# Performance work log

Hardware: AMD Instinct MI355X
Metric: run time of the kernel (lower is better)

Reference implementation:

```python
import jax, jax.numpy as jnp
import numpy as np

N, E, G = 50000, 500000, 2048
HID, H, ED, L = 128, 4, 12, 8
D = HID // H
EPS_BN = 1e-5


def setup_inputs() -> dict:
    key = jax.random.key(0)
    ks = jax.random.split(key, 32)
    s = 0.05
    x = jax.random.normal(ks[0], (N, 22), jnp.float32)
    src = jax.random.randint(ks[1], (E,), 0, N)
    off = jax.random.randint(ks[2], (E,), 1, N)
    dst = (src + off) % N  # guaranteed no self-loops -> move_mask is all True
    batch = jnp.sort(jax.random.randint(ks[3], (N,), 0, G))
    edge_attr = jax.random.normal(ks[4], (E, ED), jnp.float32)
    params = dict(
        Win=jax.random.normal(ks[5], (22, HID), jnp.float32) * s,
        b_in=jnp.zeros((HID,), jnp.float32),
        Wl=jax.random.normal(ks[6], (L, HID, HID), jnp.float32) * s,
        bl=jnp.zeros((L, HID), jnp.float32),
        Wr=jax.random.normal(ks[7], (L, HID, HID), jnp.float32) * s,
        br=jnp.zeros((L, HID), jnp.float32),
        We=jax.random.normal(ks[8], (L, ED, HID), jnp.float32) * s,
        att=jax.random.normal(ks[9], (L, H, D), jnp.float32) * s,
        bo=jnp.zeros((L, HID), jnp.float32),
        gamma=jnp.ones((L, HID), jnp.float32),
        beta=jnp.zeros((L, HID), jnp.float32),
        Wv1=jax.random.normal(ks[10], (HID, 64), jnp.float32) * s,
        bv1=jnp.zeros((64,), jnp.float32),
        Wv2=jax.random.normal(ks[11], (64, 3), jnp.float32) * s,
        bv2=jnp.zeros((3,), jnp.float32),
        Wp1=jax.random.normal(ks[12], (2 * HID + ED, 64), jnp.float32) * s,
        bp1=jnp.zeros((64,), jnp.float32),
        Wp2=jax.random.normal(ks[13], (64, 1), jnp.float32) * s,
        bp2=jnp.zeros((1,), jnp.float32),
    )
    return dict(x=x, src=src, dst=dst, batch=batch, edge_attr=edge_attr, **params)


def _bn(h, g, b):
    mu = h.mean(0)
    var = h.var(0)
    return (h - mu) * jax.lax.rsqrt(var + EPS_BN) * g + b


def _gatv2(h, src, dst, edge_attr, Wl, bl, Wr, br, We, att, bo):
    xl = (h @ Wl + bl).reshape(N, H, D)   # source-side (values + score)
    xr = (h @ Wr + br).reshape(N, H, D)   # target-side (score)
    e = (edge_attr @ We).reshape(E, H, D)
    sc = xl[src] + xr[dst] + e            # [E,H,D]
    sc = jnp.where(sc > 0, sc, 0.2 * sc)  # LeakyReLU(0.2)
    a = jnp.einsum('ehd,hd->eh', sc, att)  # [E,H]
    m = jax.ops.segment_max(a, dst, num_segments=N)
    ex = jnp.exp(a - m[dst])
    den = jax.ops.segment_sum(ex, dst, num_segments=N)
    alpha = ex / (den[dst] + 1e-16)        # per-destination softmax
    out = jax.ops.segment_sum(xl[src] * alpha[..., None], dst, num_segments=N)
    return out.reshape(N, HID) + bo


def reference(x, src, dst, batch, edge_attr, Win, b_in, Wl, bl, Wr, br, We, att,
              bo, gamma, beta, Wv1, bv1, Wv2, bv2, Wp1, bp1, Wp2, bp2):
    h = jax.nn.relu(x @ Win + b_in)
    for blk in range(L // 2):
        i, j = 2 * blk, 2 * blk + 1
        res = h
        h = jax.nn.relu(_bn(_gatv2(h, src, dst, edge_attr, Wl[i], bl[i], Wr[i], br[i], We[i], att[i], bo[i]), gamma[i], beta[i]))
        h = _bn(_gatv2(h, src, dst, edge_attr, Wl[j], bl[j], Wr[j], br[j], We[j], att[j], bo[j]), gamma[j], beta[j])
        h = jax.nn.relu(h + res)
    cnt = jax.ops.segment_sum(jnp.ones((N,), h.dtype), batch, num_segments=G)
    pooled = jax.ops.segment_sum(h, batch, num_segments=G) / jnp.maximum(cnt, 1.0)[:, None]
    value_logits = jax.nn.relu(pooled @ Wv1 + bv1) @ Wv2 + bv2   # [G,3]
    edge_in = jnp.concatenate([h[src], h[dst], edge_attr], axis=1)  # [E, 2*HID+ED]
    policy_logits = (jax.nn.relu(edge_in @ Wp1 + bp1) @ Wp2 + bp2)[:, 0]  # [E]
    return (value_logits, policy_logits)
```

## Files before the change

kernel.cpp:

```cpp
#include <hip/hip_runtime.h>
#include <math.h>

#define N_NODES 50000
#define N_EDGES 500000
#define N_GRAPHS 2048
#define HID 128
#define EDIM 12
#define NLAYERS 8
#define EPS_BN 1e-5f
#define LOG2E 1.44269504088896340736f

typedef __attribute__((ext_vector_type(8))) short short8;
typedef __attribute__((ext_vector_type(4))) float f32x4;
typedef __attribute__((ext_vector_type(2))) float f32x2;
typedef unsigned int uint;
typedef unsigned short ushort;

__device__ inline ushort f2bf(float x) {
  unsigned u = __float_as_uint(x);
  u = (u + 0x7FFFu + ((u >> 16) & 1u)) >> 16;
  return (ushort)u;
}
__device__ inline unsigned pk_bf16(float a, float b) {
  return (unsigned)f2bf(a) | ((unsigned)f2bf(b) << 16);
}
__device__ inline float bflo(uint q) { return __uint_as_float(q << 16); }
__device__ inline float bfhi(uint q) { return __uint_as_float(q & 0xFFFF0000u); }
__device__ inline f32x2 pfma(f32x2 a, f32x2 b, f32x2 c) {
  return __builtin_elementwise_fma(a, b, c);
}
template <int CTRL>
__device__ inline float dpp_add(float v) {
  int s = __builtin_amdgcn_update_dpp(0, __float_as_int(v), CTRL, 0xF, 0xF, true);
  return v + __int_as_float(s);
}
#define RED16(v)              \
  v = dpp_add<0xB1>(v);       \
  v = dpp_add<0x4E>(v);       \
  v = dpp_add<0x141>(v);      \
  v = dpp_add<0x140>(v);

__global__ void zero_kernel(int* deg, int* cursor, float* stats, uint* erec) {
  int i = blockIdx.x * 256 + threadIdx.x;
  if (i < N_NODES) { deg[i] = 0; cursor[i] = 0; }
  if (i < NLAYERS * 256) stats[i] = 0.f;
  if (i < 32) erec[(size_t)N_EDGES * 8 + i] = 0u;
}

__global__ void count_kernel(const int* __restrict__ dst, int* __restrict__ deg) {
  int e = blockIdx.x * 256 + threadIdx.x;
  if (e < N_EDGES) atomicAdd(&deg[dst[e]], 1);
}

__global__ void scan1_kernel(int* __restrict__ off, int* __restrict__ bsum) {
  __shared__ int s[256];
  int t = threadIdx.x; int n = blockIdx.x * 256 + t;
  int x = (n < N_NODES) ? off[n] : 0;
  s[t] = x; __syncthreads();
  for (int o = 1; o < 256; o <<= 1) {
    int v = (t >= o) ? s[t - o] : 0;
    __syncthreads(); s[t] += v; __syncthreads();
  }
  if (n < N_NODES) off[n] = s[t] - x;
  if (t == 255) bsum[blockIdx.x] = s[255];
}

__global__ void scan2_kernel(int* __restrict__ bsum, int nb) {
  __shared__ int s[256];
  int t = threadIdx.x;
  int x = (t < nb) ? bsum[t] : 0;
  s[t] = x; __syncthreads();
  for (int o = 1; o < 256; o <<= 1) {
    int v = (t >= o) ? s[t - o] : 0;
    __syncthreads(); s[t] += v; __syncthreads();
  }
  if (t < nb) bsum[t] = s[t] - x;
}

__global__ void scan3_kernel(int* __restrict__ off, const int* __restrict__ bsum) {
  int t = threadIdx.x; int n = blockIdx.x * 256 + t;
  if (n < N_NODES) off[n] += bsum[blockIdx.x];
  if (n == 0 && blockIdx.x == 0) off[N_NODES] = N_EDGES;
}

__global__ void scatter_kernel(const int* __restrict__ src, const int* __restrict__ dst,
                               const float* __restrict__ ea,
                               const int* __restrict__ off, int* __restrict__ cursor,
                               uint* __restrict__ erec) {
  int e = blockIdx.x * 256 + threadIdx.x;
  if (e < N_EDGES) {
    int d = dst[e];
    int p = atomicAdd(&cursor[d], 1);
    int pos = off[d] + p;
    const float* eap = &ea[(size_t)e * EDIM];
    float4 e0 = *(const float4*)eap;
    float4 e1 = *(const float4*)(eap + 4);
    float4 e2 = *(const float4*)(eap + 8);
    uint4 q0, q1;
    q0.x = (uint)src[e]; q0.y = 0u;
    q0.z = pk_bf16(e0.x, e0.y); q0.w = pk_bf16(e0.z, e0.w);
    q1.x = pk_bf16(e1.x, e1.y); q1.y = pk_bf16(e1.z, e1.w);
    q1.z = pk_bf16(e2.x, e2.y); q1.w = pk_bf16(e2.z, e2.w);
    uint* o = &erec[(size_t)pos * 8];
    *(uint4*)o = q0;
    *(uint4*)(o + 4) = q1;
  }
}

__global__ void wprep_kernel(const float* __restrict__ Wl, const float* __restrict__ Wr,
                             ushort* __restrict__ wpk) {
  int idx = blockIdx.x * 256 + threadIdx.x;
  if (idx >= NLAYERS * 4 * 256 * 32) return;
  int kk = idx & 31;
  int cc = (idx >> 5) & 255;
  int kb = (idx >> 13) & 3;
  int layer = idx >> 15;
  int k = kb * 32 + kk;
  float v = (cc < 128) ? Wl[((size_t)layer * 128 + k) * 128 + cc]
                       : Wr[((size_t)layer * 128 + k) * 128 + (cc - 128)];
  wpk[idx] = f2bf(v);
}

__global__ void wprep_pol_kernel(const float* __restrict__ Wp1, ushort* __restrict__ wppk) {
  int idx = blockIdx.x * 256 + threadIdx.x;
  if (idx >= 4 * 128 * 32) return;
  int kk = idx & 31;
  int cc = (idx >> 5) & 127;
  int kb = idx >> 12;
  int k = kb * 32 + kk;
  float v = (cc < 64) ? Wp1[(size_t)k * 64 + cc] : Wp1[(size_t)(128 + k) * 64 + (cc - 64)];
  wppk[idx] = f2bf(v);
}

__global__ void inproj_kernel(const float* __restrict__ x, const float* __restrict__ Win,
                              const float* __restrict__ b_in, float* __restrict__ h,
                              ushort* __restrict__ h16) {
  __shared__ float xs[44];
  int t = threadIdx.x;
  int n0 = blockIdx.x * 2;
  if (t < 44) xs[t] = x[n0 * 22 + t];
  __syncthreads();
  int c = t & 127, half = t >> 7;
  int n = n0 + half;
  if (n < N_NODES) {
    float acc = b_in[c];
#pragma unroll
    for (int k = 0; k < 22; k++) acc = fmaf(xs[half * 22 + k], Win[k * HID + c], acc);
    float v = fmaxf(acc, 0.f);
    h[(size_t)n * HID + c] = v;
    h16[(size_t)n * HID + c] = f2bf(v);
  }
}

template <int NOUT, int SPLIT, bool BIAS, bool OUTBF16, bool BNFUSE, bool RESID, bool WRITEH>
__global__ __launch_bounds__(256) void gemm_mfma_kernel(
    const ushort* __restrict__ A16, const ushort* __restrict__ T16,
    const float* __restrict__ stats, const float* __restrict__ gamma,
    const float* __restrict__ beta, const float* __restrict__ res,
    float* __restrict__ hout,
    const ushort* __restrict__ Wpk, const float* __restrict__ b1,
    const float* __restrict__ b2, void* __restrict__ C1v, void* __restrict__ C2v,
    int nrows) {
  __shared__ ushort As[64][136];
  int t = threadIdx.x;
  int brow = blockIdx.x * 64;
  if constexpr (!BNFUSE) {
#pragma unroll
    for (int i = 0; i < 4; i++) {
      int f = t + i * 256;
      int r = f >> 4, cg = (f & 15) * 8;
      int g = brow + r;
      uint4 v = make_uint4(0, 0, 0, 0);
      if (g < nrows) v = *(const uint4*)&A16[(size_t)g * HID + cg];
      *(uint4*)&As[r][cg] = v;
    }
  } else {
    int cg = (t & 31) * 4;
    int r0 = t >> 5;
    const float invN = 1.f / (float)N_NODES;
    float4 sm = *(const float4*)&stats[cg];
    float4 sq = *(const float4*)&stats[128 + cg];
    float4 gm = *(const float4*)&gamma[cg];
    float4 bt = *(const float4*)&beta[cg];
    float s4[4] = {sm.x, sm.y, sm.z, sm.w};
    float q4[4] = {sq.x, sq.y, sq.z, sq.w};
    float g4[4] = {gm.x, gm.y, gm.z, gm.w};
    float bb4[4] = {bt.x, bt.y, bt.z, bt.w};
    float scl[4], shf[4];
#pragma unroll
    for (int k = 0; k < 4; k++) {
      float mu = s4[k] * invN;
      float var = q4[k] * invN - mu * mu;
      float rs = rsqrtf(var + EPS_BN);
      scl[k] = g4[k] * rs;
      shf[k] = bb4[k] - mu * scl[k];
    }
#pragma unroll
    for (int rr = 0; rr < 8; rr++) {
      int r = r0 + rr * 8;
      int g = brow + r;
      uint2 tvu = make_uint2(0u, 0u);
      if (g < nrows) tvu = *(const uint2*)&T16[(size_t)g * HID + cg];
      float o0 = fmaf(bflo(tvu.x), scl[0], shf[0]);
      float o1 = fmaf(bfhi(tvu.x), scl[1], shf[1]);
      float o2 = fmaf(bflo(tvu.y), scl[2], shf[2]);
      float o3 = fmaf(bfhi(tvu.y), scl[3], shf[3]);
      if constexpr (RESID) {
        if (g < nrows) {
          float4 rv = *(const float4*)&res[(size_t)g * HID + cg];
          o0 += rv.x; o1 += rv.y; o2 += rv.z; o3 += rv.w;
        }
      }
      o0 = fmaxf(o0, 0.f); o1 = fmaxf(o1, 0.f);
      o2 = fmaxf(o2, 0.f); o3 = fmaxf(o3, 0.f);
      if constexpr (WRITEH) {
        if (g < nrows) {
          float4 ov = make_float4(o0, o1, o2, o3);
          *(float4*)&hout[(size_t)g * HID + cg] = ov;
        }
      }
      *(uint2*)&As[r][cg] = make_uint2(pk_bf16(o0, o1), pk_bf16(o2, o3));
    }
  }
  __syncthreads();
  int lane = t & 63, wave = t >> 6;
  int arow = wave * 16 + (lane & 15);
  int k8 = (lane >> 4) * 8;
  constexpr int NT = NOUT / 16;
  f32x4 acc[NT];
#pragma unroll
  for (int n = 0; n < NT; n++) acc[n] = (f32x4){0.f, 0.f, 0.f, 0.f};
#pragma unroll
  for (int kb = 0; kb < 4; kb++) {
    short8 a = *(const short8*)&As[arow][kb * 32 + k8];
#pragma unroll
    for (int n = 0; n < NT; n++) {
      int col = n * 16 + (lane & 15);
      short8 b = *(const short8*)&Wpk[((size_t)(kb * NOUT + col)) * 32 + k8];
      acc[n] = __builtin_amdgcn_mfma_f32_16x16x32_bf16(a, b, acc[n], 0, 0, 0);
    }
  }
  int rbase = brow + wave * 16 + (lane >> 4) * 4;
  int ccol = lane & 15;
#pragma unroll
  for (int n = 0; n < NT; n++) {
    int col = n * 16 + ccol;
    float bias = 0.f;
    if (BIAS) bias = (col < SPLIT) ? b1[col] : b2[col - SPLIT];
    int colw = (col < SPLIT) ? col : col - SPLIT;
#pragma unroll
    for (int j = 0; j < 4; j++) {
      int row = rbase + j;
      if (row < nrows) {
        float v = acc[n][j] + bias;
        if (OUTBF16) {
          ushort* dstp = (ushort*)((col < SPLIT) ? C1v : C2v);
          dstp[(size_t)row * SPLIT + colw] = f2bf(v);
        } else {
          float* dstp = (float*)((col < SPLIT) ? C1v : C2v);
          dstp[(size_t)row * SPLIT + colw] = v;
        }
      }
    }
  }
}

#define GAT_EDGE(ra, rb, xlw, m, d, acc)                                    \
  {                                                                         \
    f32x2 xa = (f32x2){bflo(xlw), bfhi(xlw)};                               \
    f32x2 ep = xa + xrv;                                                    \
    uint q;                                                                 \
    q = ra.z;                                                               \
    ep = pfma((f32x2){bflo(q), bflo(q)}, wk[0], ep);                        \
    ep = pfma((f32x2){bfhi(q), bfhi(q)}, wk[1], ep);                        \
    q = ra.w;                                                               \
    ep = pfma((f32x2){bflo(q), bflo(q)}, wk[2], ep);                        \
    ep = pfma((f32x2){bfhi(q), bfhi(q)}, wk[3], ep);                        \
    q = rb.x;                                                               \
    ep = pfma((f32x2){bflo(q), bflo(q)}, wk[4], ep);                        \
    ep = pfma((f32x2){bfhi(q), bfhi(q)}, wk[5], ep);                        \
    q = rb.y;                                                               \
    ep = pfma((f32x2){bflo(q), bflo(q)}, wk[6], ep);                        \
    ep = pfma((f32x2){bfhi(q), bfhi(q)}, wk[7], ep);                        \
    q = rb.z;                                                               \
    ep = pfma((f32x2){bflo(q), bflo(q)}, wk[8], ep);                        \
    ep = pfma((f32x2){bfhi(q), bfhi(q)}, wk[9], ep);                        \
    q = rb.w;                                                               \
    ep = pfma((f32x2){bflo(q), bflo(q)}, wk[10], ep);                       \
    ep = pfma((f32x2){bfhi(q), bfhi(q)}, wk[11], ep);                       \
    f32x2 sv = __builtin_elementwise_max(ep, ep * (f32x2){0.2f, 0.2f});     \
    float v = fmaf(sv.y, at.y, sv.x * at.x);                                \
    RED16(v)                                                                \
    float dm = v - m;                                                       \
    float e = __builtin_amdgcn_exp2f(-fabsf(dm));                           \
    bool big = dm > 0.f;                                                    \
    float sc = big ? e : 1.f;                                               \
    float p = big ? 1.f : e;                                                \
    m = fmaxf(m, v);                                                        \
    d = fmaf(d, sc, p);                                                     \
    acc = pfma(acc, (f32x2){sc, sc}, (f32x2){p, p} * xa);                   \
  }

__global__ __launch_bounds__(256, 4) void gat_kernel(
    const ushort* __restrict__ xl16, const ushort* __restrict__ xr16,
    const uint* __restrict__ erec, const int* __restrict__ off,
    const float* __restrict__ Wel, const float* __restrict__ attl,
    const float* __restrict__ bol, ushort* __restrict__ out16) {
  int lane = threadIdx.x & 63;
  int node = blockIdx.x * 4 + (threadIdx.x >> 6);
  if (node >= N_NODES) return;
  int c0 = lane * 2;

  f32x2 wk[12];
#pragma unroll
  for (int k = 0; k < 12; k++) {
    float2 w = *(const float2*)&Wel[k * HID + c0];
    wk[k] = (f32x2){w.x, w.y};
  }
  float2 at = *(const float2*)&attl[c0];
  at.x *= LOG2E; at.y *= LOG2E;
  uint xrd = *(const uint*)&xr16[((uint)node << 7) + c0];
  f32x2 xrv = (f32x2){bflo(xrd), bfhi(xrd)};

  int is = off[node], deg = off[node + 1] - is;
  const uint* p = erec + (size_t)is * 8;

  float m0 = -INFINITY, d0 = 0.f;
  float m1 = -INFINITY, d1 = 0.f;
  f32x2 acc0 = (f32x2){0.f, 0.f};
  f32x2 acc1 = (f32x2){0.f, 0.f};

  if (deg > 0) {
    uint4 Aa = *(const uint4*)p,        Ab = *(const uint4*)(p + 4);
    uint4 Ba = *(const uint4*)(p + 8),  Bb = *(const uint4*)(p + 12);
    uint xA = *(const uint*)&xl16[(Aa.x << 7) + c0];
    int i = 0;
    for (; i + 2 <= deg; i += 2) {
      uint xB = *(const uint*)&xl16[(Ba.x << 7) + c0];
      const uint* q2 = p + (size_t)(i + 2) * 8;
      uint4 Ca = *(const uint4*)q2,        Cb = *(const uint4*)(q2 + 4);
      uint4 Da = *(const uint4*)(q2 + 8),  Db = *(const uint4*)(q2 + 12);
      GAT_EDGE(Aa, Ab, xA, m0, d0, acc0)
      uint xC = *(const uint*)&xl16[(Ca.x << 7) + c0];
      GAT_EDGE(Ba, Bb, xB, m1, d1, acc1)
      Aa = Ca; Ab = Cb; Ba = Da; Bb = Db; xA = xC;
    }
    if (i < deg) GAT_EDGE(Aa, Ab, xA, m0, d0, acc0)
  }
  float mn = fmaxf(m0, m1);
  float w0 = (m0 > -INFINITY) ? __builtin_amdgcn_exp2f(m0 - mn) : 0.f;
  float w1 = (m1 > -INFINITY) ? __builtin_amdgcn_exp2f(m1 - mn) : 0.f;
  float den = d0 * w0 + d1 * w1;
  f32x2 acc = acc0 * (f32x2){w0, w0} + acc1 * (f32x2){w1, w1};
  float inv = 1.f / (den + 1e-16f);
  float2 bo2 = *(const float2*)&bol[c0];
  out16[((uint)node << 7) + c0 + 0] = f2bf(fmaf(acc.x, inv, bo2.x));
  out16[((uint)node << 7) + c0 + 1] = f2bf(fmaf(acc.y, inv, bo2.y));
}

__global__ void bnstats_kernel(const ushort* __restrict__ t16, float* __restrict__ sums) {
  int tid = threadIdx.x;
  int c2 = (tid & 63) * 2;
  int grp = tid >> 6;
  float s0 = 0.f, s1 = 0.f, q0 = 0.f, q1 = 0.f;
  for (int n = blockIdx.x * 4 + grp; n < N_NODES; n += 1024) {
    uint v = *(const uint*)&t16[((uint)n << 7) + c2];
    float a = bflo(v), b = bfhi(v);
    s0 += a; q0 = fmaf(a, a, q0);
    s1 += b; q1 = fmaf(b, b, q1);
  }
  __shared__ float ls[4][128], lq[4][128];
  *(float2*)&ls[grp][c2] = make_float2(s0, s1);
  *(float2*)&lq[grp][c2] = make_float2(q0, q1);
  __syncthreads();
  if (tid < 128) {
    float s = ls[0][tid] + ls[1][tid] + ls[2][tid] + ls[3][tid];
    atomicAdd(&sums[tid], s);
    float q = lq[0][tid] + lq[1][tid] + lq[2][tid] + lq[3][tid];
    atomicAdd(&sums[128 + tid], q);
  }
}

__global__ __launch_bounds__(256) void policy_kernel(
    const ushort* __restrict__ Ps, const ushort* __restrict__ Pd,
    const int* __restrict__ src, const int* __restrict__ dst,
    const float* __restrict__ edge_attr, const float* __restrict__ Wp1e,
    const float* __restrict__ bp1, const float* __restrict__ Wp2,
    const float* __restrict__ bp2, float* __restrict__ outp) {
  int lane = threadIdx.x & 63;
  int j = lane & 15;
  int e = (blockIdx.x * 256 + threadIdx.x) >> 4;
  if (e >= N_EDGES) return;
  float4 we[12];
#pragma unroll
  for (int k = 0; k < 12; k++) we[k] = *(const float4*)&Wp1e[k * 64 + j * 4];
  float4 b4 = *(const float4*)&bp1[j * 4];
  float4 w2 = *(const float4*)&Wp2[j * 4];
  float bp2c = bp2[0];
  int s = src[e], d = dst[e];
  const float* eap = &edge_attr[(size_t)e * EDIM];
  float4 e0 = *(const float4*)eap;
  float4 e1 = *(const float4*)(eap + 4);
  float4 e2 = *(const float4*)(eap + 8);
  uint2 psu = *(const uint2*)&Ps[(size_t)s * 64 + j * 4];
  uint2 pdu = *(const uint2*)&Pd[(size_t)d * 64 + j * 4];
  float eav[12] = {e0.x, e0.y, e0.z, e0.w, e1.x, e1.y, e1.z, e1.w, e2.x, e2.y, e2.z, e2.w};
  float hx = bflo(psu.x) + bflo(pdu.x) + b4.x;
  float hy = bfhi(psu.x) + bfhi(pdu.x) + b4.y;
  float hz = bflo(psu.y) + bflo(pdu.y) + b4.z;
  float hw = bfhi(psu.y) + bfhi(pdu.y) + b4.w;
#pragma unroll
  for (int k = 0; k < 12; k++) {
    hx = fmaf(eav[k], we[k].x, hx);
    hy = fmaf(eav[k], we[k].y, hy);
    hz = fmaf(eav[k], we[k].z, hz);
    hw = fmaf(eav[k], we[k].w, hw);
  }
  hx = fmaxf(hx, 0.f); hy = fmaxf(hy, 0.f); hz = fmaxf(hz, 0.f); hw = fmaxf(hw, 0.f);
  float v = fmaf(hx, w2.x, fmaf(hy, w2.y, fmaf(hz, w2.z, hw * w2.w)));
  v += __shfl_xor(v, 1);
  v += __shfl_xor(v, 2);
  v += __shfl_xor(v, 4);
  v += __shfl_xor(v, 8);
  if (j == 0) outp[e] = v + bp2c;
}

__device__ int lower_bound_dev(const int* a, int n, int key) {
  int lo = 0, hi = n;
  while (lo < hi) {
    int mid = (lo + hi) >> 1;
    if (a[mid] < key) lo = mid + 1; else hi = mid;
  }
  return lo;
}

__global__ void poolvalue_kernel(const float* __restrict__ h, const int* __restrict__ batch,
                                 const float* __restrict__ Wv1, const float* __restrict__ bv1,
                                 const float* __restrict__ Wv2, const float* __restrict__ bv2,
                                 float* __restrict__ outv) {
  __shared__ float pl[128];
  __shared__ float hd[64];
  __shared__ int range[2];
  int g = blockIdx.x, t = threadIdx.x;
  if (t == 0) {
    range[0] = lower_bound_dev(batch, N_NODES, g);
    range[1] = lower_bound_dev(batch, N_NODES, g + 1);
  }
  __syncthreads();
  int lo = range[0], hi = range[1];
  float s = 0.f;
  for (int n = lo; n < hi; n++) s += h[(size_t)n * HID + t];
  float cnt = (float)(hi - lo);
  pl[t] = s / fmaxf(cnt, 1.f);
  __syncthreads();
  if (t < 64) {
    float a = bv1[t];
    for (int c = 0; c < 128; c++) a = fmaf(pl[c], Wv1[c * 64 + t], a);
    hd[t] = fmaxf(a, 0.f);
  }
  __syncthreads();
  if (t < 3) {
    float a = bv2[t];
    for (int j = 0; j < 64; j++) a = fmaf(hd[j], Wv2[j * 3 + t], a);
    outv[g * 3 + t] = a;
  }
}

extern "C" void kernel_launch(void* const* d_in, const int* in_sizes, int n_in,
                              void* d_out, int out_size, void* d_ws, size_t ws_size,
                              hipStream_t stream) {
  (void)in_sizes; (void)n_in; (void)out_size; (void)ws_size;
  const float* x    = (const float*)d_in[0];
  const int*   src  = (const int*)d_in[1];
  const int*   dst  = (const int*)d_in[2];
  const int*   batch= (const int*)d_in[3];
  const float* ea   = (const float*)d_in[4];
  const float* Win  = (const float*)d_in[5];
  const float* b_in = (const float*)d_in[6];
  const float* Wl   = (const float*)d_in[7];
  const float* bl   = (const float*)d_in[8];
  const float* Wr   = (const float*)d_in[9];
  const float* br   = (const float*)d_in[10];
  const float* We   = (const float*)d_in[11];
  const float* att  = (const float*)d_in[12];
  const float* bo   = (const float*)d_in[13];
  const float* gamma= (const float*)d_in[14];
  const float* beta = (const float*)d_in[15];
  const float* Wv1  = (const float*)d_in[16];
  const float* bv1  = (const float*)d_in[17];
  const float* Wv2  = (const float*)d_in[18];
  const float* bv2  = (const float*)d_in[19];
  const float* Wp1  = (const float*)d_in[20];
  const float* bp1  = (const float*)d_in[21];
  const float* Wp2  = (const float*)d_in[22];
  const float* bp2  = (const float*)d_in[23];

  float* outv = (float*)d_out;
  float* outp = outv + (size_t)N_GRAPHS * 3;

  float* hres   = (float*)d_ws;
  ushort* tmp16 = (ushort*)(hres + (size_t)N_NODES * HID);
  ushort* h16   = tmp16 + (size_t)N_NODES * HID;
  ushort* xl16  = h16 + (size_t)N_NODES * HID;
  ushort* xr16  = xl16 + (size_t)N_NODES * HID;
  float* stats  = (float*)(xr16 + (size_t)N_NODES * HID);
  ushort* wpk   = (ushort*)(stats + NLAYERS * 256);
  ushort* wppk  = wpk + (size_t)NLAYERS * 4 * 256 * 32;
  int* off    = (int*)(wppk + 4 * 128 * 32);
  int* cursor = off + (N_NODES + 1);
  int* bsum   = cursor + N_NODES;
  uint* erec  = (uint*)(((uintptr_t)(bsum + 256) + 15) & ~(uintptr_t)15);

  const int NB = (N_NODES + 255) / 256;
  const int EB = (N_EDGES + 255) / 256;

  zero_kernel<<<NB, 256, 0, stream>>>(off, cursor, stats, erec);
  count_kernel<<<EB, 256, 0, stream>>>(dst, off);
  scan1_kernel<<<NB, 256, 0, stream>>>(off, bsum);
  scan2_kernel<<<1, 256, 0, stream>>>(bsum, NB);
  scan3_kernel<<<NB, 256, 0, stream>>>(off, bsum);
  scatter_kernel<<<EB, 256, 0, stream>>>(src, dst, ea, off, cursor, erec);
  wprep_kernel<<<(NLAYERS * 4 * 256 * 32 + 255) / 256, 256, 0, stream>>>(Wl, Wr, wpk);
  wprep_pol_kernel<<<(4 * 128 * 32 + 255) / 256, 256, 0, stream>>>(Wp1, wppk);
  inproj_kernel<<<N_NODES / 2, 256, 0, stream>>>(x, Win, b_in, hres, h16);

  const int MB = (N_NODES + 63) / 64;
  const int GATB = (N_NODES + 3) / 4;

  for (int l = 0; l < NLAYERS; l++) {
    if (l == 0) {
      gemm_mfma_kernel<256, 128, true, true, false, false, false><<<MB, 256, 0, stream>>>(
          h16, nullptr, nullptr, nullptr, nullptr, nullptr, nullptr,
          wpk, bl, br, xl16, xr16, N_NODES);
    } else if (l & 1) {
      int p = l - 1;
      gemm_mfma_kernel<256, 128, true, true, true, false, false><<<MB, 256, 0, stream>>>(
          nullptr, tmp16, stats + p * 256, gamma + p * HID, beta + p * HID, nullptr, nullptr,
          wpk + (size_t)l * 32768, bl + l * HID, br + l * HID, xl16, xr16, N_NODES);
    } else {
      int p = l - 1;
      gemm_mfma_kernel<256, 128, true, true, true, true, true><<<MB, 256, 0, stream>>>(
          nullptr, tmp16, stats + p * 256, gamma + p * HID, beta + p * HID, hres, hres,
          wpk + (size_t)l * 32768, bl + l * HID, br + l * HID, xl16, xr16, N_NODES);
    }
    gat_kernel<<<GATB, 256, 0, stream>>>(xl16, xr16, erec, off,
                                         We + (size_t)l * EDIM * HID, att + (size_t)l * HID,
                                         bo + (size_t)l * HID, tmp16);
    bnstats_kernel<<<256, 256, 0, stream>>>(tmp16, stats + l * 256);
  }

  ushort* Ps = xl16;
  ushort* Pd = xr16;
  gemm_mfma_kernel<128, 64, false, true, true, true, true><<<MB, 256, 0, stream>>>(
      nullptr, tmp16, stats + 7 * 256, gamma + 7 * HID, beta + 7 * HID, hres, hres,
      wppk, nullptr, nullptr, Ps, Pd, N_NODES);
  policy_kernel<<<(N_EDGES + 15) / 16, 256, 0, stream>>>(Ps, Pd, src, dst, ea,
                                                         Wp1 + 256 * 64, bp1, Wp2, bp2, outp);
  poolvalue_kernel<<<N_GRAPHS, 128, 0, stream>>>(hres, batch, Wv1, bv1, Wv2, bv2, outv);
}
```

Baseline: 1.296 ms.

## Split GAT edges across wavefront halves and make policy kernel grid-stride

The GAT aggregation kernel now gives each half of a 64-lane wavefront a separate edge stream (even and odd edges). Each lane handles four channels instead of two, and the two partial online-softmax states are merged with cross-half shuffles at the end. This halves the per-node serial edge loop and shortens the attention-score reduction to 8 lanes, at the cost of more registers per lane and a masked tail edge. Separately, the policy kernel becomes a persistent grid-stride loop over 2048 blocks, so the per-thread weight loads are amortised across many edges.

```diff
diff --git a/kernel.cpp b/kernel.cpp
--- a/kernel.cpp
+++ b/kernel.cpp
@@ -34,11 +34,10 @@
   int s = __builtin_amdgcn_update_dpp(0, __float_as_int(v), CTRL, 0xF, 0xF, true);
   return v + __int_as_float(s);
 }
-#define RED16(v)              \
+#define RED8(v)               \
   v = dpp_add<0xB1>(v);       \
   v = dpp_add<0x4E>(v);       \
-  v = dpp_add<0x141>(v);      \
-  v = dpp_add<0x140>(v);
+  v = dpp_add<0x141>(v);
 
 __global__ void zero_kernel(int* deg, int* cursor, float* stats, uint* erec) {
   int i = blockIdx.x * 256 + threadIdx.x;
@@ -265,40 +264,58 @@
   }
 }
 
-#define GAT_EDGE(ra, rb, xlw, m, d, acc)                                    \
-  {                                                                         \
-    f32x2 xa = (f32x2){bflo(xlw), bfhi(xlw)};                               \
-    f32x2 ep = xa + xrv;                                                    \
-    uint q;                                                                 \
-    q = ra.z;                                                               \
-    ep = pfma((f32x2){bflo(q), bflo(q)}, wk[0], ep);                        \
-    ep = pfma((f32x2){bfhi(q), bfhi(q)}, wk[1], ep);                        \
-    q = ra.w;                                                               \
-    ep = pfma((f32x2){bflo(q), bflo(q)}, wk[2], ep);                        \
-    ep = pfma((f32x2){bfhi(q), bfhi(q)}, wk[3], ep);                        \
-    q = rb.x;                                                               \
-    ep = pfma((f32x2){bflo(q), bflo(q)}, wk[4], ep);                        \
-    ep = pfma((f32x2){bfhi(q), bfhi(q)}, wk[5], ep);                        \
-    q = rb.y;                                                               \
-    ep = pfma((f32x2){bflo(q), bflo(q)}, wk[6], ep);                        \
-    ep = pfma((f32x2){bfhi(q), bfhi(q)}, wk[7], ep);                        \
-    q = rb.z;                                                               \
-    ep = pfma((f32x2){bflo(q), bflo(q)}, wk[8], ep);                        \
-    ep = pfma((f32x2){bfhi(q), bfhi(q)}, wk[9], ep);                        \
-    q = rb.w;                                                               \
-    ep = pfma((f32x2){bflo(q), bflo(q)}, wk[10], ep);                       \
-    ep = pfma((f32x2){bfhi(q), bfhi(q)}, wk[11], ep);                       \
-    f32x2 sv = __builtin_elementwise_max(ep, ep * (f32x2){0.2f, 0.2f});     \
-    float v = fmaf(sv.y, at.y, sv.x * at.x);                                \
-    RED16(v)                                                                \
-    float dm = v - m;                                                       \
-    float e = __builtin_amdgcn_exp2f(-fabsf(dm));                           \
-    bool big = dm > 0.f;                                                    \
-    float sc = big ? e : 1.f;                                               \
-    float p = big ? 1.f : e;                                                \
-    m = fmaxf(m, v);                                                        \
-    d = fmaf(d, sc, p);                                                     \
-    acc = pfma(acc, (f32x2){sc, sc}, (f32x2){p, p} * xa);                   \
+#define GAT_EDGE4(ra, rb, xw, OKEXPR)                                        \
+  {                                                                          \
+    f32x2 xa01 = (f32x2){bflo(xw.x), bfhi(xw.x)};                            \
+    f32x2 xa23 = (f32x2){bflo(xw.y), bfhi(xw.y)};                            \
+    f32x2 ep01 = xa01 + xr01;                                                \
+    f32x2 ep23 = xa23 + xr23;                                                \
+    uint q; float lo, hi;                                                    \
+    q = ra.z; lo = bflo(q); hi = bfhi(q);                                    \
+    ep01 = pfma((f32x2){lo, lo}, wk01[0], ep01);                             \
+    ep23 = pfma((f32x2){lo, lo}, wk23[0], ep23);                             \
+    ep01 = pfma((f32x2){hi, hi}, wk01[1], ep01);                             \
+    ep23 = pfma((f32x2){hi, hi}, wk23[1], ep23);                             \
+    q = ra.w; lo = bflo(q); hi = bfhi(q);                                    \
+    ep01 = pfma((f32x2){lo, lo}, wk01[2], ep01);                             \
+    ep23 = pfma((f32x2){lo, lo}, wk23[2], ep23);                             \
+    ep01 = pfma((f32x2){hi, hi}, wk01[3], ep01);                             \
+    ep23 = pfma((f32x2){hi, hi}, wk23[3], ep23);                             \
+    q = rb.x; lo = bflo(q); hi = bfhi(q);                                    \
+    ep01 = pfma((f32x2){lo, lo}, wk01[4], ep01);                             \
+    ep23 = pfma((f32x2){lo, lo}, wk23[4], ep23);                             \
+    ep01 = pfma((f32x2){hi, hi}, wk01[5], ep01);                             \
+    ep23 = pfma((f32x2){hi, hi}, wk23[5], ep23);                             \
+    q = rb.y; lo = bflo(q); hi = bfhi(q);                                    \
+    ep01 = pfma((f32x2){lo, lo}, wk01[6], ep01);                             \
+    ep23 = pfma((f32x2){lo, lo}, wk23[6], ep23);                             \
+    ep01 = pfma((f32x2){hi, hi}, wk01[7], ep01);                             \
+    ep23 = pfma((f32x2){hi, hi}, wk23[7], ep23);                             \
+    q = rb.z; lo = bflo(q); hi = bfhi(q);                                    \
+    ep01 = pfma((f32x2){lo, lo}, wk01[8], ep01);                             \
+    ep23 = pfma((f32x2){lo, lo}, wk23[8], ep23);                             \
+    ep01 = pfma((f32x2){hi, hi}, wk01[9], ep01);                             \
+    ep23 = pfma((f32x2){hi, hi}, wk23[9], ep23);                             \
+    q = rb.w; lo = bflo(q); hi = bfhi(q);                                    \
+    ep01 = pfma((f32x2){lo, lo}, wk01[10], ep01);                            \
+    ep23 = pfma((f32x2){lo, lo}, wk23[10], ep23);                            \
+    ep01 = pfma((f32x2){hi, hi}, wk01[11], ep01);                            \
+    ep23 = pfma((f32x2){hi, hi}, wk23[11], ep23);                            \
+    f32x2 s01 = __builtin_elementwise_max(ep01, ep01 * (f32x2){0.2f, 0.2f}); \
+    f32x2 s23 = __builtin_elementwise_max(ep23, ep23 * (f32x2){0.2f, 0.2f}); \
+    float v = fmaf(s01.x, at4.x,                                             \
+              fmaf(s01.y, at4.y, fmaf(s23.x, at4.z, s23.y * at4.w)));        \
+    RED8(v)                                                                  \
+    bool ok = (OKEXPR);                                                      \
+    float dm = v - m;                                                        \
+    float e = __builtin_amdgcn_exp2f(-fabsf(dm));                            \
+    bool big = dm > 0.f;                                                     \
+    float sc = (big && ok) ? e : 1.f;                                        \
+    float p = ok ? (big ? 1.f : e) : 0.f;                                    \
+    m = (ok && big) ? v : m;                                                 \
+    d = fmaf(d, sc, p);                                                      \
+    acc01 = pfma(acc01, (f32x2){sc, sc}, (f32x2){p, p} * xa01);              \
+    acc23 = pfma(acc23, (f32x2){sc, sc}, (f32x2){p, p} * xa23);              \
   }
 
 __global__ __launch_bounds__(256, 4) void gat_kernel(
@@ -309,53 +326,62 @@
   int lane = threadIdx.x & 63;
   int node = blockIdx.x * 4 + (threadIdx.x >> 6);
   if (node >= N_NODES) return;
-  int c0 = lane * 2;
-
-  f32x2 wk[12];
+  int half = lane >> 5;
+  int c0 = (lane & 31) * 4;
+
+  f32x2 wk01[12], wk23[12];
 #pragma unroll
   for (int k = 0; k < 12; k++) {
-    float2 w = *(const float2*)&Wel[k * HID + c0];
-    wk[k] = (f32x2){w.x, w.y};
-  }
-  float2 at = *(const float2*)&attl[c0];
-  at.x *= LOG2E; at.y *= LOG2E;
-  uint xrd = *(const uint*)&xr16[((uint)node << 7) + c0];
-  f32x2 xrv = (f32x2){bflo(xrd), bfhi(xrd)};
+    float4 w = *(const float4*)&Wel[k * HID + c0];
+    wk01[k] = (f32x2){w.x, w.y};
+    wk23[k] = (f32x2){w.z, w.w};
+  }
+  float4 at4 = *(const float4*)&attl[c0];
+  at4.x *= LOG2E; at4.y *= LOG2E; at4.z *= LOG2E; at4.w *= LOG2E;
+  uint2 xru = *(const uint2*)&xr16[((uint)node << 7) + c0];
+  f32x2 xr01 = (f32x2){bflo(xru.x), bfhi(xru.x)};
+  f32x2 xr23 = (f32x2){bflo(xru.y), bfhi(xru.y)};
 
   int is = off[node], deg = off[node + 1] - is;
-  const uint* p = erec + (size_t)is * 8;
-
-  float m0 = -INFINITY, d0 = 0.f;
-  float m1 = -INFINITY, d1 = 0.f;
-  f32x2 acc0 = (f32x2){0.f, 0.f};
-  f32x2 acc1 = (f32x2){0.f, 0.f};
+
+  float m = -INFINITY, d = 0.f;
+  f32x2 acc01 = (f32x2){0.f, 0.f};
+  f32x2 acc23 = (f32x2){0.f, 0.f};
 
   if (deg > 0) {
-    uint4 Aa = *(const uint4*)p,        Ab = *(const uint4*)(p + 4);
-    uint4 Ba = *(const uint4*)(p + 8),  Bb = *(const uint4*)(p + 12);
-    uint xA = *(const uint*)&xl16[(Aa.x << 7) + c0];
-    int i = 0;
-    for (; i + 2 <= deg; i += 2) {
-      uint xB = *(const uint*)&xl16[(Ba.x << 7) + c0];
-      const uint* q2 = p + (size_t)(i + 2) * 8;
-      uint4 Ca = *(const uint4*)q2,        Cb = *(const uint4*)(q2 + 4);
-      uint4 Da = *(const uint4*)(q2 + 8),  Db = *(const uint4*)(q2 + 12);
-      GAT_EDGE(Aa, Ab, xA, m0, d0, acc0)
-      uint xC = *(const uint*)&xl16[(Ca.x << 7) + c0];
-      GAT_EDGE(Ba, Bb, xB, m1, d1, acc1)
-      Aa = Ca; Ab = Cb; Ba = Da; Bb = Db; xA = xC;
-    }
-    if (i < deg) GAT_EDGE(Aa, Ab, xA, m0, d0, acc0)
-  }
-  float mn = fmaxf(m0, m1);
-  float w0 = (m0 > -INFINITY) ? __builtin_amdgcn_exp2f(m0 - mn) : 0.f;
-  float w1 = (m1 > -INFINITY) ? __builtin_amdgcn_exp2f(m1 - mn) : 0.f;
-  float den = d0 * w0 + d1 * w1;
-  f32x2 acc = acc0 * (f32x2){w0, w0} + acc1 * (f32x2){w1, w1};
+    const uint* pe = erec + ((size_t)is + half) * 8;
+    uint4 Ra = *(const uint4*)pe, Rb = *(const uint4*)(pe + 4);
+    uint2 xw = *(const uint2*)&xl16[(Ra.x << 7) + c0];
+    int full = deg >> 1;
+    for (int i = 0; i < full; i++) {
+      const uint* pn = pe + 16;
+      uint4 Na = *(const uint4*)pn, Nb = *(const uint4*)(pn + 4);
+      uint2 xn = *(const uint2*)&xl16[(Na.x << 7) + c0];
+      GAT_EDGE4(Ra, Rb, xw, true)
+      Ra = Na; Rb = Nb; xw = xn; pe = pn;
+    }
+    if (deg & 1) GAT_EDGE4(Ra, Rb, xw, half == 0)
+  }
+
+  float mo = __shfl_xor(m, 32);
+  float dd = __shfl_xor(d, 32);
+  f32x2 o01, o23;
+  o01.x = __shfl_xor(acc01.x, 32); o01.y = __shfl_xor(acc01.y, 32);
+  o23.x = __shfl_xor(acc23.x, 32); o23.y = __shfl_xor(acc23.y, 32);
+  float mn = fmaxf(m, mo);
+  float wS = (m > -INFINITY) ? __builtin_amdgcn_exp2f(m - mn) : 0.f;
+  float wO = (mo > -INFINITY) ? __builtin_amdgcn_exp2f(mo - mn) : 0.f;
+  float den = d * wS + dd * wO;
+  f32x2 a01 = acc01 * (f32x2){wS, wS} + o01 * (f32x2){wO, wO};
+  f32x2 a23 = acc23 * (f32x2){wS, wS} + o23 * (f32x2){wO, wO};
   float inv = 1.f / (den + 1e-16f);
-  float2 bo2 = *(const float2*)&bol[c0];
-  out16[((uint)node << 7) + c0 + 0] = f2bf(fmaf(acc.x, inv, bo2.x));
-  out16[((uint)node << 7) + c0 + 1] = f2bf(fmaf(acc.y, inv, bo2.y));
+  if (half == 0) {
+    float4 bo = *(const float4*)&bol[c0];
+    uint2 o;
+    o.x = pk_bf16(fmaf(a01.x, inv, bo.x), fmaf(a01.y, inv, bo.y));
+    o.y = pk_bf16(fmaf(a23.x, inv, bo.z), fmaf(a23.y, inv, bo.w));
+    *(uint2*)&out16[((uint)node << 7) + c0] = o;
+  }
 }
 
 __global__ void bnstats_kernel(const ushort* __restrict__ t16, float* __restrict__ sums) {
@@ -387,42 +413,43 @@
     const float* __restrict__ edge_attr, const float* __restrict__ Wp1e,
     const float* __restrict__ bp1, const float* __restrict__ Wp2,
     const float* __restrict__ bp2, float* __restrict__ outp) {
-  int lane = threadIdx.x & 63;
-  int j = lane & 15;
-  int e = (blockIdx.x * 256 + threadIdx.x) >> 4;
-  if (e >= N_EDGES) return;
+  int j = threadIdx.x & 15;
+  int gid = (blockIdx.x * 256 + threadIdx.x) >> 4;
+  int ngroups = (gridDim.x * 256) >> 4;
   float4 we[12];
 #pragma unroll
   for (int k = 0; k < 12; k++) we[k] = *(const float4*)&Wp1e[k * 64 + j * 4];
   float4 b4 = *(const float4*)&bp1[j * 4];
   float4 w2 = *(const float4*)&Wp2[j * 4];
   float bp2c = bp2[0];
-  int s = src[e], d = dst[e];
-  const float* eap = &edge_attr[(size_t)e * EDIM];
-  float4 e0 = *(const float4*)eap;
-  float4 e1 = *(const float4*)(eap + 4);
-  float4 e2 = *(const float4*)(eap + 8);
-  uint2 psu = *(const uint2*)&Ps[(size_t)s * 64 + j * 4];
-  uint2 pdu = *(const uint2*)&Pd[(size_t)d * 64 + j * 4];
-  float eav[12] = {e0.x, e0.y, e0.z, e0.w, e1.x, e1.y, e1.z, e1.w, e2.x, e2.y, e2.z, e2.w};
-  float hx = bflo(psu.x) + bflo(pdu.x) + b4.x;
-  float hy = bfhi(psu.x) + bfhi(pdu.x) + b4.y;
-  float hz = bflo(psu.y) + bflo(pdu.y) + b4.z;
-  float hw = bfhi(psu.y) + bfhi(pdu.y) + b4.w;
-#pragma unroll
-  for (int k = 0; k < 12; k++) {
-    hx = fmaf(eav[k], we[k].x, hx);
-    hy = fmaf(eav[k], we[k].y, hy);
-    hz = fmaf(eav[k], we[k].z, hz);
-    hw = fmaf(eav[k], we[k].w, hw);
-  }
-  hx = fmaxf(hx, 0.f); hy = fmaxf(hy, 0.f); hz = fmaxf(hz, 0.f); hw = fmaxf(hw, 0.f);
-  float v = fmaf(hx, w2.x, fmaf(hy, w2.y, fmaf(hz, w2.z, hw * w2.w)));
-  v += __shfl_xor(v, 1);
-  v += __shfl_xor(v, 2);
-  v += __shfl_xor(v, 4);
-  v += __shfl_xor(v, 8);
-  if (j == 0) outp[e] = v + bp2c;
+  for (int e = gid; e < N_EDGES; e += ngroups) {
+    int s = src[e], d = dst[e];
+    const float* eap = &edge_attr[(size_t)e * EDIM];
+    float4 e0 = *(const float4*)eap;
+    float4 e1 = *(const float4*)(eap + 4);
+    float4 e2 = *(const float4*)(eap + 8);
+    uint2 psu = *(const uint2*)&Ps[(size_t)s * 64 + j * 4];
+    uint2 pdu = *(const uint2*)&Pd[(size_t)d * 64 + j * 4];
+    float eav[12] = {e0.x, e0.y, e0.z, e0.w, e1.x, e1.y, e1.z, e1.w, e2.x, e2.y, e2.z, e2.w};
+    float hx = bflo(psu.x) + bflo(pdu.x) + b4.x;
+    float hy = bfhi(psu.x) + bfhi(pdu.x) + b4.y;
+    float hz = bflo(psu.y) + bflo(pdu.y) + b4.z;
+    float hw = bfhi(psu.y) + bfhi(pdu.y) + b4.w;
+#pragma unroll
+    for (int k = 0; k < 12; k++) {
+      hx = fmaf(eav[k], we[k].x, hx);
+      hy = fmaf(eav[k], we[k].y, hy);
+      hz = fmaf(eav[k], we[k].z, hz);
+      hw = fmaf(eav[k], we[k].w, hw);
+    }
+    hx = fmaxf(hx, 0.f); hy = fmaxf(hy, 0.f); hz = fmaxf(hz, 0.f); hw = fmaxf(hw, 0.f);
+    float v = fmaf(hx, w2.x, fmaf(hy, w2.y, fmaf(hz, w2.z, hw * w2.w)));
+    v += __shfl_xor(v, 1);
+    v += __shfl_xor(v, 2);
+    v += __shfl_xor(v, 4);
+    v += __shfl_xor(v, 8);
+    if (j == 0) outp[e] = v + bp2c;
+  }
 }
 
 __device__ int lower_bound_dev(const int* a, int n, int key) {
@@ -554,7 +581,7 @@
   gemm_mfma_kernel<128, 64, false, true, true, true, true><<<MB, 256, 0, stream>>>(
       nullptr, tmp16, stats + 7 * 256, gamma + 7 * HID, beta + 7 * HID, hres, hres,
       wppk, nullptr, nullptr, Ps, Pd, N_NODES);
-  policy_kernel<<<(N_EDGES + 15) / 16, 256, 0, stream>>>(Ps, Pd, src, dst, ea,
-                                                         Wp1 + 256 * 64, bp1, Wp2, bp2, outp);
+  policy_kernel<<<2048, 256, 0, stream>>>(Ps, Pd, src, dst, ea,
+                                          Wp1 + 256 * 64, bp1, Wp2, bp2, outp);
   poolvalue_kernel<<<N_GRAPHS, 128, 0, stream>>>(hres, batch, Wv1, bv1, Wv2, bv2, outv);
 }
```

After: 1.240 ms. 4.3% less time.
